# Kernel optimization log

Measured on AMD Instinct MI355X. Metric: run time of the kernel, lower is better.

The kernel has to match this reference:

```python
import jax, jax.numpy as jnp
import numpy as np

B, NR, M, NL = 1, 384, 4, 128
IN_C, MID_C, OUT_C = 384, 32, 128


def setup_inputs() -> dict:
    key = jax.random.key(0)
    ks = jax.random.split(key, 24)
    s = 0.02
    d = {
        'rec_1d': jax.random.normal(ks[0], (B, NR, IN_C), jnp.float32),
        'lig_1d': jax.random.normal(ks[1], (B, M, NL, IN_C), jnp.float32),
        'pw_rep': jax.random.normal(ks[2], (B, NR + NL, NR + NL, OUT_C), jnp.float32),
        'rl1_w': jax.random.normal(ks[3], (MID_C, IN_C), jnp.float32) * s,
        'rl1_b': jax.random.normal(ks[4], (MID_C,), jnp.float32) * s,
        'rl2_w': jax.random.normal(ks[5], (MID_C, IN_C), jnp.float32) * s,
        'rl2_b': jax.random.normal(ks[6], (MID_C,), jnp.float32) * s,
        'll1_w': jax.random.normal(ks[7], (MID_C, IN_C), jnp.float32) * s,
        'll1_b': jax.random.normal(ks[8], (MID_C,), jnp.float32) * s,
        'll2_w': jax.random.normal(ks[9], (MID_C, IN_C), jnp.float32) * s,
        'll2_b': jax.random.normal(ks[10], (MID_C,), jnp.float32) * s,
        'rr_w': jax.random.normal(ks[11], (OUT_C, MID_C * MID_C), jnp.float32) * s,
        'rr_b': jax.random.normal(ks[12], (OUT_C,), jnp.float32) * s,
        'rl_w': jax.random.normal(ks[13], (OUT_C, MID_C * MID_C), jnp.float32) * s,
        'rl_b': jax.random.normal(ks[14], (OUT_C,), jnp.float32) * s,
        'lr_w': jax.random.normal(ks[15], (OUT_C, MID_C * MID_C), jnp.float32) * s,
        'lr_b': jax.random.normal(ks[16], (OUT_C,), jnp.float32) * s,
        'll_w': jax.random.normal(ks[17], (OUT_C, MID_C * MID_C), jnp.float32) * s,
        'll_b': jax.random.normal(ks[18], (OUT_C,), jnp.float32) * s,
    }
    return d


def reference(rec_1d, lig_1d, pw_rep,
              rl1_w, rl1_b, rl2_w, rl2_b,
              ll1_w, ll1_b, ll2_w, ll2_b,
              rr_w, rr_b, rl_w, rl_b, lr_w, lr_b, ll_w, ll_b):
    mid_c = rl1_w.shape[0]
    m = lig_1d.shape[1]

    # 1D projections (nn.Linear: x @ W.T + b)
    r_i = rec_1d @ rl1_w.T + rl1_b          # [b, NR, mid]
    r_j = rec_1d @ rl2_w.T + rl2_b          # [b, NR, mid]
    l_i = lig_1d @ ll1_w.T + ll1_b          # [b, m, NL, mid]
    l_j = lig_1d @ ll2_w.T + ll2_b          # [b, m, NL, mid]

    # final Linear weights over flattened (x, y) -> [out, x, y] (y fastest, matching .view)
    Wrr = rr_w.reshape(-1, mid_c, mid_c)
    Wrl = rl_w.reshape(-1, mid_c, mid_c)
    Wlr = lr_w.reshape(-1, mid_c, mid_c)
    Wll = ll_w.reshape(-1, mid_c, mid_c)

    # rr[b,i,j,o] = sum_xy r_i[b,i,x] r_j[b,j,y] Wrr[o,x,y]
    # contract projection weight with one factor first (OpenFold trick):
    rr = jnp.einsum('bioy,bjy->bijo', jnp.einsum('bix,oxy->bioy', r_i, Wrr), r_j) + rr_b

    # mean over m commutes with the broadcast outer products for rl/lr
    l_j_mean = l_j.mean(axis=1)             # [b, NL, mid]
    l_i_mean = l_i.mean(axis=1)             # [b, NL, mid]

    rl = jnp.einsum('bioy,bjy->bijo', jnp.einsum('bix,oxy->bioy', r_i, Wrl), l_j_mean) + rl_b

    # lr output is [b, j_lig, i_res, o]: x-axis from r_j, y-axis from l_i
    lr = jnp.einsum('bioy,bjy->bjio', jnp.einsum('bix,oxy->bioy', r_j, Wlr), l_i_mean) + lr_b

    # ll: mean over m of per-copy outer products (not separable)
    ll = jnp.einsum('bmioy,bmjy->bijo', jnp.einsum('bmix,oxy->bmioy', l_i, Wll), l_j) / m + ll_b

    top = jnp.concatenate([rr, rl], axis=2)  # [b, NR, NR+NL, out]
    bot = jnp.concatenate([lr, ll], axis=2)  # [b, NL, NR+NL, out]
    pw_update = jnp.concatenate([top, bot], axis=1).astype(pw_rep.dtype)
    return pw_update
```

## Files before the change

kernel.cpp:

```cpp
#include <hip/hip_runtime.h>

#define NRES 384
#define NLIG 128
#define INC 384
#define OUTC 128
#define NTOT 512

#define WS_RI   0
#define WS_RJ   12288
#define WS_LI   24576
#define WS_LJ   40960
#define WS_BF16 57344

#define BT_RR   0
#define BT_RL   1572864
#define BT_LR   3145728
#define BT_LL   4718592
#define BF_RJ   6815744
#define BF_LJM  6828032
#define BF_LIM  6832128
#define BF_LJ   6836224
#define BF_RI   6852608
#define BF_LI   6864896
#define BW_W    6881280

typedef __bf16 bf16x8 __attribute__((ext_vector_type(8)));
typedef float  f32x4  __attribute__((ext_vector_type(4)));

__device__ inline bf16x8 cvt8(const float* p) {
  f32x4 a = *(const f32x4*)p, b = *(const f32x4*)(p + 4);
  bf16x8 r;
  r[0] = (__bf16)a[0]; r[1] = (__bf16)a[1]; r[2] = (__bf16)a[2]; r[3] = (__bf16)a[3];
  r[4] = (__bf16)b[0]; r[5] = (__bf16)b[1]; r[6] = (__bf16)b[2]; r[7] = (__bf16)b[3];
  return r;
}

__global__ __launch_bounds__(256) void kP_proj(
    const float* __restrict__ rec, const float* __restrict__ lig,
    const float* __restrict__ rl1w, const float* __restrict__ rl1b,
    const float* __restrict__ rl2w, const float* __restrict__ rl2b,
    const float* __restrict__ ll1w, const float* __restrict__ ll1b,
    const float* __restrict__ ll2w, const float* __restrict__ ll2b,
    const float* __restrict__ Wrr, const float* __restrict__ Wrl,
    const float* __restrict__ Wlr, const float* __restrict__ Wll,
    float* __restrict__ ws) {
  int b = blockIdx.x, t = threadIdx.x;
  __bf16* B16 = (__bf16*)(ws + WS_BF16);
  if (b >= 28) {
    int bb = b - 28;
    int tt = bb >> 2, oc = bb & 3;
    const float* W = tt == 0 ? Wrr : tt == 1 ? Wrl : tt == 2 ? Wlr : Wll;
    __bf16* Wb = B16 + BW_W + tt * 131072;
    int nbase = oc * 1024;
#pragma unroll
    for (int kk = 0; kk < 128; ++kk) {
      int idx = kk * 256 + t;
      int nl = idx >> 5, x = idx & 31;
      int o = (oc * 32) + (nl >> 5), y = nl & 31;
      Wb[(size_t)(nbase + nl) * 32 + x] = (__bf16)W[(size_t)o * 1024 + x * 32 + y];
    }
    return;
  }
  int l = t & 63, w = t >> 6;
  int lr16 = l & 15, lq = l >> 4;
  int pair = w >> 1, rh = w & 1;

  const float* in;
  const float *w1, *b1, *w2, *b2;
  float *o1, *o2;
  __bf16 *bf1, *bf2;
  int row0;
  if (b < 12) {
    row0 = b * 32;
    in = rec; w1 = rl1w; b1 = rl1b; w2 = rl2w; b2 = rl2b;
    o1 = ws + WS_RI; o2 = ws + WS_RJ;
    bf1 = B16 + BF_RI; bf2 = B16 + BF_RJ;
  } else {
    row0 = (b - 12) * 32;
    in = lig; w1 = ll1w; b1 = ll1b; w2 = ll2w; b2 = ll2b;
    o1 = ws + WS_LI; o2 = ws + WS_LJ;
    bf1 = B16 + BF_LI; bf2 = B16 + BF_LJ;
  }
  const float* wsrc = pair ? w2 : w1;
  const float* bsrc = pair ? b2 : b1;
  float* osrc = pair ? o2 : o1;
  __bf16* bdst = pair ? bf2 : bf1;
  int arow = row0 + rh * 16 + lr16;

  f32x4 acc[2];
#pragma unroll
  for (int ci = 0; ci < 2; ++ci) acc[ci] = (f32x4){0.f, 0.f, 0.f, 0.f};
  for (int ks = 0; ks < 12; ++ks) {
    bf16x8 af = cvt8(in + (size_t)arow * INC + ks * 32 + lq * 8);
#pragma unroll
    for (int ci = 0; ci < 2; ++ci) {
      int ch = ci * 16 + lr16;
      bf16x8 bf = cvt8(wsrc + (size_t)ch * INC + ks * 32 + lq * 8);
      acc[ci] = __builtin_amdgcn_mfma_f32_16x16x32_bf16(af, bf, acc[ci], 0, 0, 0);
    }
  }
#pragma unroll
  for (int ci = 0; ci < 2; ++ci) {
    int c = ci * 16 + lr16;
    float bias = bsrc[c];
#pragma unroll
    for (int e = 0; e < 4; ++e) {
      int r = row0 + rh * 16 + 4 * lq + e;
      float v = acc[ci][e] + bias;
      osrc[r * 32 + c] = v;
      bdst[r * 32 + c] = (__bf16)v;
    }
  }
}

__global__ __launch_bounds__(256) void k2_makeA(float* __restrict__ ws) {
  int b = blockIdx.x, t = threadIdx.x;
  __bf16* B16 = (__bf16*)(ws + WS_BF16);
  if (b >= 128) {
    const float* lj = ws + WS_LJ;
    const float* li = ws + WS_LI;
    __bf16* dm = B16 + BF_LJM;
    __bf16* di = B16 + BF_LIM;
    for (int k = 0; k < 16; ++k) {
      int idx = k * 256 + t;
      dm[idx] = (__bf16)(0.25f * (lj[idx] + lj[4096 + idx] + lj[8192 + idx] + lj[12288 + idx]));
      di[idx] = (__bf16)(0.25f * (li[idx] + li[4096 + idx] + li[8192 + idx] + li[12288 + idx]));
    }
    return;
  }
  int tt = b >> 5, sub = b & 31;
  int nt = sub >> 1, mh = sub & 1;
  const __bf16* facB;
  __bf16* At;
  int M;
  if (tt == 0)      { facB = B16 + BF_RI; At = B16 + BT_RR; M = 384; }
  else if (tt == 1) { facB = B16 + BF_RI; At = B16 + BT_RL; M = 384; }
  else if (tt == 2) { facB = B16 + BF_RJ; At = B16 + BT_LR; M = 384; }
  else              { facB = B16 + BF_LI; At = B16 + BT_LL; M = 512; }
  const __bf16* Wb = B16 + BW_W + tt * 131072;
  int l = t & 63, w = t >> 6;
  int lr16 = l & 15, lq = l >> 4;
  int n0w = nt * 256 + w * 64;
  int mtiles = (M >> 5);
  int m0 = mh * (M >> 1);

  bf16x8 bv[4];
#pragma unroll
  for (int q = 0; q < 4; ++q)
    bv[q] = *(const bf16x8*)(Wb + (size_t)(n0w + q * 16 + lr16) * 32 + lq * 8);

  for (int mt = 0; mt < mtiles; ++mt) {
    bf16x8 af = *(const bf16x8*)(facB + (size_t)(m0 + mt * 16 + lr16) * 32 + lq * 8);
    f32x4 acc[4];
#pragma unroll
    for (int q = 0; q < 4; ++q) acc[q] = (f32x4){0.f, 0.f, 0.f, 0.f};
#pragma unroll
    for (int q = 0; q < 4; ++q)
      acc[q] = __builtin_amdgcn_mfma_f32_16x16x32_bf16(af, bv[q], acc[q], 0, 0, 0);
#pragma unroll
    for (int q = 0; q < 4; ++q)
#pragma unroll
      for (int e = 0; e < 4; ++e)
        At[(size_t)(m0 + mt * 16 + 4 * lq + e) * 4096 + n0w + q * 16 + lr16] = (__bf16)acc[q][e];
  }
}

__global__ __launch_bounds__(256) void k3_mfma(
    const float* __restrict__ ws, float* __restrict__ out,
    const float* __restrict__ rrb, const float* __restrict__ rlb,
    const float* __restrict__ lrb, const float* __restrict__ llb) {
  const __bf16* B16 = (const __bf16*)(ws + WS_BF16);
  int b = blockIdx.x, t = threadIdx.x;
  int l = t & 63, w = t >> 6;
  int lr16 = l & 15, lq = l >> 4;

  if (b < 1920) {
    const __bf16* At;
    const __bf16* fc;
    const float* bias;
    float* outp;
    size_t jstr;
    if (b < 1152) {
      int i = b / 3, jt = b - 3 * i;
      At = B16 + BT_RR + (size_t)i * 4096;
      fc = B16 + BF_RJ + jt * 4096;
      bias = rrb; outp = out + ((size_t)i * NTOT + jt * 128) * OUTC; jstr = OUTC;
    } else if (b < 1536) {
      int i = b - 1152;
      At = B16 + BT_RL + (size_t)i * 4096;
      fc = B16 + BF_LJM;
      bias = rlb; outp = out + ((size_t)i * NTOT + NRES) * OUTC; jstr = OUTC;
    } else {
      int i = b - 1536;
      At = B16 + BT_LR + (size_t)i * 4096;
      fc = B16 + BF_LIM;
      bias = lrb; outp = out + (size_t)NRES * NTOT * OUTC + (size_t)i * OUTC;
      jstr = (size_t)NTOT * OUTC;
    }
    bf16x8 af[2];
#pragma unroll
    for (int jj = 0; jj < 2; ++jj)
      af[jj] = *(const bf16x8*)(fc + (size_t)(w * 32 + jj * 16 + lr16) * 32 + lq * 8);
    f32x4 acc[2][8];
#pragma unroll
    for (int jj = 0; jj < 2; ++jj)
#pragma unroll
      for (int ot = 0; ot < 8; ++ot) acc[jj][ot] = (f32x4){0.f, 0.f, 0.f, 0.f};
#pragma unroll
    for (int oc = 0; oc < 2; ++oc) {
      bf16x8 bv[4];
#pragma unroll
      for (int o4 = 0; o4 < 4; ++o4)
        bv[o4] = *(const bf16x8*)(At + (size_t)((oc * 4 + o4) * 16 + lr16) * 32 + lq * 8);
#pragma unroll
      for (int jj = 0; jj < 2; ++jj)
#pragma unroll
        for (int o4 = 0; o4 < 4; ++o4)
          acc[jj][oc * 4 + o4] =
              __builtin_amdgcn_mfma_f32_16x16x32_bf16(af[jj], bv[o4], acc[jj][oc * 4 + o4], 0, 0, 0);
    }
#pragma unroll
    for (int jj = 0; jj < 2; ++jj)
#pragma unroll
      for (int ot = 0; ot < 8; ++ot) {
        int col = ot * 16 + lr16;
        float bb = bias[col];
#pragma unroll
        for (int e = 0; e < 4; ++e) {
          int row = w * 32 + jj * 16 + 4 * lq + e;
          outp[(size_t)row * jstr + col] = acc[jj][ot][e] + bb;
        }
      }
  } else {
    int il = b - 1920;
    f32x4 acc[2][8];
#pragma unroll
    for (int jj = 0; jj < 2; ++jj)
#pragma unroll
      for (int ot = 0; ot < 8; ++ot) acc[jj][ot] = (f32x4){0.f, 0.f, 0.f, 0.f};
    for (int m = 0; m < 4; ++m) {
      const __bf16* At = B16 + BT_LL + (size_t)(m * 128 + il) * 4096;
      const __bf16* fc = B16 + BF_LJ + m * 4096;
      bf16x8 af[2];
#pragma unroll
      for (int jj = 0; jj < 2; ++jj)
        af[jj] = *(const bf16x8*)(fc + (size_t)(w * 32 + jj * 16 + lr16) * 32 + lq * 8);
#pragma unroll
      for (int oc = 0; oc < 2; ++oc) {
        bf16x8 bv[4];
#pragma unroll
        for (int o4 = 0; o4 < 4; ++o4)
          bv[o4] = *(const bf16x8*)(At + (size_t)((oc * 4 + o4) * 16 + lr16) * 32 + lq * 8);
#pragma unroll
        for (int jj = 0; jj < 2; ++jj)
#pragma unroll
          for (int o4 = 0; o4 < 4; ++o4)
            acc[jj][oc * 4 + o4] =
                __builtin_amdgcn_mfma_f32_16x16x32_bf16(af[jj], bv[o4], acc[jj][oc * 4 + o4], 0, 0, 0);
      }
    }
    float* outp = out + ((size_t)(NRES + il) * NTOT + NRES) * OUTC;
#pragma unroll
    for (int jj = 0; jj < 2; ++jj)
#pragma unroll
      for (int ot = 0; ot < 8; ++ot) {
        int col = ot * 16 + lr16;
        float bb = llb[col];
#pragma unroll
        for (int e = 0; e < 4; ++e) {
          int row = w * 32 + jj * 16 + 4 * lq + e;
          outp[(size_t)row * OUTC + col] = 0.25f * acc[jj][ot][e] + bb;
        }
      }
  }
}

extern "C" void kernel_launch(void* const* d_in, const int* in_sizes, int n_in,
                              void* d_out, int out_size, void* d_ws, size_t ws_size,
                              hipStream_t stream) {
  const float* rec  = (const float*)d_in[0];
  const float* lig  = (const float*)d_in[1];
  const float* rl1w = (const float*)d_in[3];
  const float* rl1b = (const float*)d_in[4];
  const float* rl2w = (const float*)d_in[5];
  const float* rl2b = (const float*)d_in[6];
  const float* ll1w = (const float*)d_in[7];
  const float* ll1b = (const float*)d_in[8];
  const float* ll2w = (const float*)d_in[9];
  const float* ll2b = (const float*)d_in[10];
  const float* rrw  = (const float*)d_in[11];
  const float* rrb  = (const float*)d_in[12];
  const float* rlw  = (const float*)d_in[13];
  const float* rlb  = (const float*)d_in[14];
  const float* lrw  = (const float*)d_in[15];
  const float* lrb  = (const float*)d_in[16];
  const float* llw  = (const float*)d_in[17];
  const float* llb  = (const float*)d_in[18];
  float* out = (float*)d_out;
  float* ws  = (float*)d_ws;

  hipLaunchKernelGGL(kP_proj, dim3(44), dim3(256), 0, stream,
                     rec, lig, rl1w, rl1b, rl2w, rl2b, ll1w, ll1b, ll2w, ll2b,
                     rrw, rlw, lrw, llw, ws);
  hipLaunchKernelGGL(k2_makeA, dim3(129), dim3(256), 0, stream, ws);
  hipLaunchKernelGGL(k3_mfma, dim3(2048), dim3(256), 0, stream,
                     ws, out, rrb, rlb, lrb, llb);
}
```

Measured before the change: 62.47 us.

## Swap MFMA operands for vectorized stores and LDS-transpose weight conversion

The MFMA A/B operands in k2 and k3 are swapped so each lane holds four consecutive output channels. That lets the output and intermediate writes become 16-byte float4 and 8-byte bf16x4 vector stores instead of scattered scalar stores. The weight transpose-to-bf16 step now goes through a padded LDS tile, which gives coalesced global reads and writes, and it is spread over 64 blocks instead of 16. The cost is extra shared memory for all kP_proj blocks and a barrier in the weight blocks.

```diff
diff --git a/kernel.cpp b/kernel.cpp
--- a/kernel.cpp
+++ b/kernel.cpp
@@ -25,6 +25,7 @@
 #define BW_W    6881280
 
 typedef __bf16 bf16x8 __attribute__((ext_vector_type(8)));
+typedef __bf16 bf16x4 __attribute__((ext_vector_type(4)));
 typedef float  f32x4  __attribute__((ext_vector_type(4)));
 
 __device__ inline bf16x8 cvt8(const float* p) {
@@ -35,6 +36,7 @@
   return r;
 }
 
+#define KW_STR 257
 __global__ __launch_bounds__(256) void kP_proj(
     const float* __restrict__ rec, const float* __restrict__ lig,
     const float* __restrict__ rl1w, const float* __restrict__ rl1b,
@@ -44,20 +46,28 @@
     const float* __restrict__ Wrr, const float* __restrict__ Wrl,
     const float* __restrict__ Wlr, const float* __restrict__ Wll,
     float* __restrict__ ws) {
+  __shared__ float lds[32 * KW_STR];
   int b = blockIdx.x, t = threadIdx.x;
   __bf16* B16 = (__bf16*)(ws + WS_BF16);
   if (b >= 28) {
     int bb = b - 28;
-    int tt = bb >> 2, oc = bb & 3;
+    int tt = bb >> 4, oc = bb & 15;
     const float* W = tt == 0 ? Wrr : tt == 1 ? Wrl : tt == 2 ? Wlr : Wll;
     __bf16* Wb = B16 + BW_W + tt * 131072;
-    int nbase = oc * 1024;
-#pragma unroll
-    for (int kk = 0; kk < 128; ++kk) {
-      int idx = kk * 256 + t;
-      int nl = idx >> 5, x = idx & 31;
-      int o = (oc * 32) + (nl >> 5), y = nl & 31;
-      Wb[(size_t)(nbase + nl) * 32 + x] = (__bf16)W[(size_t)o * 1024 + x * 32 + y];
+    int o0 = oc * 8;
+#pragma unroll
+    for (int it = 0; it < 32; ++it) {
+      int idx = it * 256 + t;
+      int oo = idx >> 10, r = idx & 1023;
+      int x = r >> 5, y = r & 31;
+      lds[x * KW_STR + oo * 32 + y] = W[(size_t)(o0 + oo) * 1024 + r];
+    }
+    __syncthreads();
+#pragma unroll
+    for (int it = 0; it < 32; ++it) {
+      int idx = it * 256 + t;
+      int x = idx & 31, nl = idx >> 5;
+      Wb[(size_t)(o0 * 32 + nl) * 32 + x] = (__bf16)lds[x * KW_STR + nl];
     }
     return;
   }
@@ -144,24 +154,27 @@
   int mtiles = (M >> 5);
   int m0 = mh * (M >> 1);
 
-  bf16x8 bv[4];
+  bf16x8 wv[4];
 #pragma unroll
   for (int q = 0; q < 4; ++q)
-    bv[q] = *(const bf16x8*)(Wb + (size_t)(n0w + q * 16 + lr16) * 32 + lq * 8);
+    wv[q] = *(const bf16x8*)(Wb + (size_t)(n0w + q * 16 + lr16) * 32 + lq * 8);
 
   for (int mt = 0; mt < mtiles; ++mt) {
-    bf16x8 af = *(const bf16x8*)(facB + (size_t)(m0 + mt * 16 + lr16) * 32 + lq * 8);
+    bf16x8 fv = *(const bf16x8*)(facB + (size_t)(m0 + mt * 16 + lr16) * 32 + lq * 8);
     f32x4 acc[4];
 #pragma unroll
     for (int q = 0; q < 4; ++q) acc[q] = (f32x4){0.f, 0.f, 0.f, 0.f};
 #pragma unroll
     for (int q = 0; q < 4; ++q)
-      acc[q] = __builtin_amdgcn_mfma_f32_16x16x32_bf16(af, bv[q], acc[q], 0, 0, 0);
-#pragma unroll
-    for (int q = 0; q < 4; ++q)
-#pragma unroll
-      for (int e = 0; e < 4; ++e)
-        At[(size_t)(m0 + mt * 16 + 4 * lq + e) * 4096 + n0w + q * 16 + lr16] = (__bf16)acc[q][e];
+      acc[q] = __builtin_amdgcn_mfma_f32_16x16x32_bf16(wv[q], fv, acc[q], 0, 0, 0);
+    int m = m0 + mt * 16 + lr16;
+#pragma unroll
+    for (int q = 0; q < 4; ++q) {
+      bf16x4 v;
+#pragma unroll
+      for (int e = 0; e < 4; ++e) v[e] = (__bf16)acc[q][e];
+      *(bf16x4*)(At + (size_t)m * 4096 + n0w + q * 16 + 4 * lq) = v;
+    }
   }
 }
 
@@ -197,10 +210,10 @@
       bias = lrb; outp = out + (size_t)NRES * NTOT * OUTC + (size_t)i * OUTC;
       jstr = (size_t)NTOT * OUTC;
     }
-    bf16x8 af[2];
+    bf16x8 fj[2];
 #pragma unroll
     for (int jj = 0; jj < 2; ++jj)
-      af[jj] = *(const bf16x8*)(fc + (size_t)(w * 32 + jj * 16 + lr16) * 32 + lq * 8);
+      fj[jj] = *(const bf16x8*)(fc + (size_t)(w * 32 + jj * 16 + lr16) * 32 + lq * 8);
     f32x4 acc[2][8];
 #pragma unroll
     for (int jj = 0; jj < 2; ++jj)
@@ -208,29 +221,27 @@
       for (int ot = 0; ot < 8; ++ot) acc[jj][ot] = (f32x4){0.f, 0.f, 0.f, 0.f};
 #pragma unroll
     for (int oc = 0; oc < 2; ++oc) {
-      bf16x8 bv[4];
+      bf16x8 av[4];
 #pragma unroll
       for (int o4 = 0; o4 < 4; ++o4)
-        bv[o4] = *(const bf16x8*)(At + (size_t)((oc * 4 + o4) * 16 + lr16) * 32 + lq * 8);
+        av[o4] = *(const bf16x8*)(At + (size_t)((oc * 4 + o4) * 16 + lr16) * 32 + lq * 8);
 #pragma unroll
       for (int jj = 0; jj < 2; ++jj)
 #pragma unroll
         for (int o4 = 0; o4 < 4; ++o4)
           acc[jj][oc * 4 + o4] =
-              __builtin_amdgcn_mfma_f32_16x16x32_bf16(af[jj], bv[o4], acc[jj][oc * 4 + o4], 0, 0, 0);
-    }
-#pragma unroll
-    for (int jj = 0; jj < 2; ++jj)
+              __builtin_amdgcn_mfma_f32_16x16x32_bf16(av[o4], fj[jj], acc[jj][oc * 4 + o4], 0, 0, 0);
+    }
+#pragma unroll
+    for (int jj = 0; jj < 2; ++jj) {
+      int j = w * 32 + jj * 16 + lr16;
 #pragma unroll
       for (int ot = 0; ot < 8; ++ot) {
-        int col = ot * 16 + lr16;
-        float bb = bias[col];
-#pragma unroll
-        for (int e = 0; e < 4; ++e) {
-          int row = w * 32 + jj * 16 + 4 * lq + e;
-          outp[(size_t)row * jstr + col] = acc[jj][ot][e] + bb;
-        }
+        f32x4 b4 = *(const f32x4*)&bias[ot * 16 + 4 * lq];
+        f32x4 v = acc[jj][ot] + b4;
+        *(f32x4*)&outp[(size_t)j * jstr + ot * 16 + 4 * lq] = v;
       }
+    }
   } else {
     int il = b - 1920;
     f32x4 acc[2][8];
@@ -241,37 +252,35 @@
     for (int m = 0; m < 4; ++m) {
       const __bf16* At = B16 + BT_LL + (size_t)(m * 128 + il) * 4096;
       const __bf16* fc = B16 + BF_LJ + m * 4096;
-      bf16x8 af[2];
+      bf16x8 fj[2];
 #pragma unroll
       for (int jj = 0; jj < 2; ++jj)
-        af[jj] = *(const bf16x8*)(fc + (size_t)(w * 32 + jj * 16 + lr16) * 32 + lq * 8);
+        fj[jj] = *(const bf16x8*)(fc + (size_t)(w * 32 + jj * 16 + lr16) * 32 + lq * 8);
 #pragma unroll
       for (int oc = 0; oc < 2; ++oc) {
-        bf16x8 bv[4];
+        bf16x8 av[4];
 #pragma unroll
         for (int o4 = 0; o4 < 4; ++o4)
-          bv[o4] = *(const bf16x8*)(At + (size_t)((oc * 4 + o4) * 16 + lr16) * 32 + lq * 8);
+          av[o4] = *(const bf16x8*)(At + (size_t)((oc * 4 + o4) * 16 + lr16) * 32 + lq * 8);
 #pragma unroll
         for (int jj = 0; jj < 2; ++jj)
 #pragma unroll
           for (int o4 = 0; o4 < 4; ++o4)
             acc[jj][oc * 4 + o4] =
-                __builtin_amdgcn_mfma_f32_16x16x32_bf16(af[jj], bv[o4], acc[jj][oc * 4 + o4], 0, 0, 0);
+                __builtin_amdgcn_mfma_f32_16x16x32_bf16(av[o4], fj[jj], acc[jj][oc * 4 + o4], 0, 0, 0);
       }
     }
     float* outp = out + ((size_t)(NRES + il) * NTOT + NRES) * OUTC;
 #pragma unroll
-    for (int jj = 0; jj < 2; ++jj)
+    for (int jj = 0; jj < 2; ++jj) {
+      int j = w * 32 + jj * 16 + lr16;
 #pragma unroll
       for (int ot = 0; ot < 8; ++ot) {
-        int col = ot * 16 + lr16;
-        float bb = llb[col];
-#pragma unroll
-        for (int e = 0; e < 4; ++e) {
-          int row = w * 32 + jj * 16 + 4 * lq + e;
-          outp[(size_t)row * OUTC + col] = 0.25f * acc[jj][ot][e] + bb;
-        }
+        f32x4 b4 = *(const f32x4*)&llb[ot * 16 + 4 * lq];
+        f32x4 v = 0.25f * acc[jj][ot] + b4;
+        *(f32x4*)&outp[(size_t)j * OUTC + ot * 16 + 4 * lq] = v;
       }
+    }
   }
 }
 
@@ -299,7 +308,7 @@
   float* out = (float*)d_out;
   float* ws  = (float*)d_ws;
 
-  hipLaunchKernelGGL(kP_proj, dim3(44), dim3(256), 0, stream,
+  hipLaunchKernelGGL(kP_proj, dim3(92), dim3(256), 0, stream,
                      rec, lig, rl1w, rl1b, rl2w, rl2b, ll1w, ll1b, ll2w, ll2b,
                      rrw, rlw, lrw, llw, ws);
   hipLaunchKernelGGL(k2_makeA, dim3(129), dim3(256), 0, stream, ws);
```

New measurement: 55.32 us. 11.4% less time.
